# Kernel tuning notes

Hardware: AMD Instinct MI355X
Metric: run time of the kernel (lower is better)

Reference implementation:

```python
import jax, jax.numpy as jnp
import numpy as np

N, E, R = 50000, 500000, 3
IN, HID, OUT = 128, 128, 128
NEG_SLOPE = 0.2


def setup_inputs() -> dict:
    key = jax.random.key(0)
    ks = jax.random.split(key, 16)
    g = lambda i, shape: jax.random.normal(ks[i], shape, jnp.float32) * 0.1
    return {
        "x": jax.random.normal(ks[0], (N, IN), jnp.float32),
        "edge_index": jax.random.randint(ks[1], (2, E), 0, N, jnp.int32),
        "edge_type": jax.random.randint(ks[2], (E,), 0, R, jnp.int32),
        "edge_attr": jax.random.normal(ks[3], (E, 1), jnp.float32),
        # conv1 params (RGATConv: per-relation weight, q/k/e attention vectors, edge lin, bias)
        "w1": g(4, (R, IN, HID)), "q1": g(5, (HID, 1)), "k1": g(6, (HID, 1)),
        "le1": g(7, (1, HID)), "e1": g(8, (HID, 1)), "b1": jnp.zeros((HID,), jnp.float32),
        # conv2 params
        "w2": g(9, (R, HID, OUT)), "q2": g(10, (OUT, 1)), "k2": g(11, (OUT, 1)),
        "le2": g(12, (1, OUT)), "e2": g(13, (OUT, 1)), "b2": jnp.zeros((OUT,), jnp.float32),
    }


def _rgat_conv(x, src, dst, edge_type, edge_attr, w, q, k, le, e, b):
    """PyG RGATConv: heads=1, dim=1, additive-self-attention, across-relation softmax."""
    n = x.shape[0]
    # Per-relation linear at node level (equiv. to per-edge bmm with w[edge_type])
    xw = jnp.einsum('ni,rio->rno', x, w)            # [R, N, C]
    x_j = xw[edge_type, src]                          # [E, C] transformed source feats
    x_i = xw[edge_type, dst]                          # [E, C] transformed target feats
    # additive attention logits: q(x_i) + k(x_j) + e(lin_edge(edge_attr))
    alpha = x_i @ q + x_j @ k + (edge_attr @ le) @ e  # [E, 1]
    alpha = jax.nn.leaky_relu(alpha, negative_slope=NEG_SLOPE)
    # across-relation softmax over incoming edges of each target node
    amax = jax.ops.segment_max(alpha, dst, num_segments=n)
    amax = jnp.where(jnp.isfinite(amax), amax, 0.0)   # empty segments -> 0
    ex = jnp.exp(alpha - amax[dst])
    denom = jax.ops.segment_sum(ex, dst, num_segments=n)
    alpha = ex / (denom[dst] + 1e-16)
    # weighted scatter-add aggregation, then bias (concat=True, heads=1)
    out = jax.ops.segment_sum(alpha * x_j, dst, num_segments=n)  # [N, C]
    return out + b


def reference(x, edge_index, edge_type, edge_attr,
              w1, q1, k1, le1, e1, b1,
              w2, q2, k2, le2, e2, b2):
    src, dst = edge_index[0], edge_index[1]
    h = jax.nn.relu(_rgat_conv(x, src, dst, edge_type, edge_attr, w1, q1, k1, le1, e1, b1))
    return _rgat_conv(h, src, dst, edge_type, edge_attr, w2, q2, k2, le2, e2, b2)
```

## Files before the change

### kernel.cpp

```cpp
#include <hip/hip_runtime.h>
#include <hip/hip_bf16.h>
#include <math.h>

typedef __bf16 bf16x8 __attribute__((ext_vector_type(8)));
typedef float f32x4 __attribute__((ext_vector_type(4)));

#define CDIM 128

__global__ void sentinel_kernel(float* outf) {
  if (threadIdx.x == 0) outf[0] = 12345.0f;
}

__global__ __launch_bounds__(256) void prep_kernel(
    const float* __restrict__ w1, const float* __restrict__ w2,
    __hip_bfloat16* __restrict__ wt,
    const float* __restrict__ le1, const float* __restrict__ e1,
    const float* __restrict__ le2, const float* __restrict__ e2,
    float* __restrict__ outc, int* __restrict__ deg, int perW, int n) {
  const int b = blockIdx.x;
  const int tid = threadIdx.x;
  if (b < 48) {
    int t = b * 256 + tid;
    if (t >= perW * 2) return;
    const float* w = (t < perW) ? w1 : w2;
    int tt = (t < perW) ? t : t - perW;
    int r = tt >> 11;
    int rem = tt & 2047;
    int kb = rem >> 7;
    int o = rem & 127;
    const float* wr = w + ((size_t)r << 14);
    union { __hip_bfloat16 h[8]; int4 v; } u;
#pragma unroll
    for (int j = 0; j < 8; ++j)
      u.h[j] = __float2bfloat16(wr[(size_t)(kb * 8 + j) * CDIM + o]);
    *reinterpret_cast<int4*>(wt + (size_t)t * 8) = u.v;
  } else if (b == 48) {
    if (tid < 64) {
      float v1 = le1[tid] * e1[tid] + le1[tid + 64] * e1[tid + 64];
      float v2 = le2[tid] * e2[tid] + le2[tid + 64] * e2[tid + 64];
#pragma unroll
      for (int off = 32; off > 0; off >>= 1) {
        v1 += __shfl_xor(v1, off, 64);
        v2 += __shfl_xor(v2, off, 64);
      }
      if (tid == 0) { outc[0] = v1; outc[1] = v2; }
    }
  } else {
    int i = (b - 49) * 256 + tid;
    if (i < n) deg[i] = 0;
  }
}


__global__ __launch_bounds__(256) void hist_kernel(const int* __restrict__ dstv,
                                                   int* __restrict__ deg, int E) {
  int e = blockIdx.x * 256 + threadIdx.x;
  if (e < E) atomicAdd(&deg[dstv[e]], 1);
}

__global__ __launch_bounds__(256) void scan1_kernel(const int* __restrict__ deg,
                                                    int* __restrict__ rowptr,
                                                    int* __restrict__ partials, int n) {
  __shared__ int sh[256];
  int t = threadIdx.x;
  int base = blockIdx.x * 1024;
  int idx = base + t * 4;
  int v[4]; int s = 0;
#pragma unroll
  for (int j = 0; j < 4; ++j) { v[j] = (idx + j < n) ? deg[idx + j] : 0; s += v[j]; }
  sh[t] = s;
  __syncthreads();
  for (int off = 1; off < 256; off <<= 1) {
    int x = (t >= off) ? sh[t - off] : 0;
    __syncthreads();
    sh[t] += x;
    __syncthreads();
  }
  int excl = sh[t] - s;
  if (t == 255) partials[blockIdx.x] = sh[255];
  int run = excl;
#pragma unroll
  for (int j = 0; j < 4; ++j) {
    if (idx + j < n) rowptr[idx + j] = run;
    run += v[j];
  }
}

__global__ __launch_bounds__(256) void scan3_kernel(int* __restrict__ rowptr,
                                                    int* __restrict__ cursor,
                                                    const int* __restrict__ partials,
                                                    int nb, int n, int E) {
  __shared__ int spfx[64];
  int t = threadIdx.x;
  if (t < 64) {
    int pv = (t < nb) ? partials[t] : 0;
    int v = pv;
#pragma unroll
    for (int off = 1; off < 64; off <<= 1) {
      int u = __shfl_up(v, off, 64);
      if (t >= off) v += u;
    }
    spfx[t] = v - pv;
  }
  __syncthreads();
  int i = blockIdx.x * 256 + t;
  if (i < n) {
    int v = rowptr[i] + spfx[i >> 10];
    rowptr[i] = v;
    cursor[i] = v;
  } else if (i == n) {
    rowptr[n] = E;
  }
}

__global__ __launch_bounds__(256) void scatter_kernel(
    const int* __restrict__ srcv, const int* __restrict__ dstv,
    const int* __restrict__ etype, const float* __restrict__ eattr,
    int* __restrict__ cursor, int2* __restrict__ kattr, int E, int n) {
  int e = blockIdx.x * 256 + threadIdx.x;
  if (e >= E) return;
  int p = atomicAdd(&cursor[dstv[e]], 1);
  kattr[p] = make_int2(etype[e] * n + srcv[e], __float_as_int(eattr[e]));
}

__global__ __launch_bounds__(256) void gemm_xw_kernel(
    const float* __restrict__ xin, const __hip_bfloat16* __restrict__ wt,
    const float* __restrict__ qv, const float* __restrict__ kv,
    __hip_bfloat16* __restrict__ xwout, float* __restrict__ sq, float* __restrict__ sk,
    int n) {
  __shared__ __hip_bfloat16 wlds[16 * 128 * 8];
  __shared__ float qls[128], kls[128];
  const int base = blockIdx.x * 64;
  const int tid = threadIdx.x;
  const int wave = tid >> 6, lane = tid & 63;
  const int quad = lane >> 4, c16 = lane & 15;

  if (tid < 128) qls[tid] = qv[tid];
  else kls[tid - 128] = kv[tid - 128];

  bf16x8 zf;
#pragma unroll
  for (int j = 0; j < 8; ++j) zf[j] = (__bf16)0.0f;

  const int m = base + wave * 16 + c16;
  const bool ok = m < n;
  bf16x8 af[4];
#pragma unroll
  for (int ks = 0; ks < 4; ++ks) {
    if (ok) {
      const float* xp = xin + (size_t)m * CDIM + ks * 32 + quad * 8;
      f32x4 x0 = *reinterpret_cast<const f32x4*>(xp);
      f32x4 x1 = *reinterpret_cast<const f32x4*>(xp + 4);
      bf16x8 a;
#pragma unroll
      for (int j = 0; j < 4; ++j) { a[j] = (__bf16)x0[j]; a[4 + j] = (__bf16)x1[j]; }
      af[ks] = a;
    } else {
      af[ks] = zf;
    }
  }

  for (int r = 0; r < 3; ++r) {
    if (r) __syncthreads();
    {
      const int4* src = reinterpret_cast<const int4*>(wt + ((size_t)r << 14));
      int4* dst = reinterpret_cast<int4*>(wlds);
#pragma unroll
      for (int i = 0; i < 8; ++i) dst[tid + i * 256] = src[tid + i * 256];
    }
    __syncthreads();

    f32x4 acc[8];
#pragma unroll
    for (int ot = 0; ot < 8; ++ot) acc[ot] = (f32x4){0.f, 0.f, 0.f, 0.f};

#pragma unroll
    for (int ks = 0; ks < 4; ++ks) {
#pragma unroll
      for (int ot = 0; ot < 8; ++ot) {
        bf16x8 b = *reinterpret_cast<const bf16x8*>(
            &wlds[(((ks * 4 + quad) * 128) + ot * 16 + c16) * 8]);
        acc[ot] = __builtin_amdgcn_mfma_f32_16x16x32_bf16(b, af[ks], acc[ot], 0, 0, 0);
      }
    }

    __hip_bfloat16* rp = xwout + (((size_t)r * n + m) << 7) + quad * 4;
    float s_q = 0.f, s_k = 0.f;
#pragma unroll
    for (int ot = 0; ot < 8; ++ot) {
      f32x4 a = acc[ot];
      f32x4 q4 = *reinterpret_cast<const f32x4*>(&qls[ot * 16 + quad * 4]);
      f32x4 k4 = *reinterpret_cast<const f32x4*>(&kls[ot * 16 + quad * 4]);
      s_q += a[0] * q4[0] + a[1] * q4[1] + a[2] * q4[2] + a[3] * q4[3];
      s_k += a[0] * k4[0] + a[1] * k4[1] + a[2] * k4[2] + a[3] * k4[3];
      if (ok) {
        union { __hip_bfloat16 b4[4]; uint2 u; } pk;
#pragma unroll
        for (int t = 0; t < 4; ++t) pk.b4[t] = __float2bfloat16(a[t]);
        *reinterpret_cast<uint2*>(rp + ot * 16) = pk.u;
      }
    }
    s_q += __shfl_xor(s_q, 16, 64);
    s_q += __shfl_xor(s_q, 32, 64);
    s_k += __shfl_xor(s_k, 16, 64);
    s_k += __shfl_xor(s_k, 32, 64);
    if (quad == 0 && ok) {
      sq[(size_t)r * n + m] = s_q;
      sk[(size_t)r * n + m] = s_k;
    }
  }
}

__global__ __launch_bounds__(256) void aggregate_kernel(
    const int* __restrict__ rowptr, const int2* __restrict__ kattr,
    const float* __restrict__ sq, const float* __restrict__ sk,
    const __hip_bfloat16* __restrict__ xw, const float* __restrict__ bias,
    const float* __restrict__ cscal, float* __restrict__ out, int n, int do_relu) {
  const int wave = threadIdx.x >> 6, lane = threadIdx.x & 63;
  const int node = blockIdx.x * 4 + wave;
  if (node >= n) return;
  const int g = lane >> 4;
  const int sub = lane & 15;
  const float c = cscal[0];
  const int n2 = n * 2;

  const int start = rowptr[node];
  const int deg = rowptr[node + 1] - start;
  const float s0 = sq[node], s1 = sq[n + node], s2 = sq[n2 + node];

  float acc[8];
#pragma unroll
  for (int t = 0; t < 8; ++t) acc[t] = 0.f;
  float den = 0.f;

  for (int j0 = 0; j0 < deg; j0 += 16) {
    const int jb = j0 + (g << 2);
    int2 ka[4];
#pragma unroll
    for (int t = 0; t < 4; ++t) {
      int idx = jb + t;
      ka[t] = kattr[start + (idx < deg ? idx : 0)];
    }
    float w[4];
    bf16x8 f[4];
#pragma unroll
    for (int t = 0; t < 4; ++t) {
      int kk = ka[t].x;
      float sv = (kk >= n2) ? s2 : ((kk >= n) ? s1 : s0);
      float l = sv + sk[kk] + c * __int_as_float(ka[t].y);
      l = l > 0.f ? l : 0.2f * l;
      w[t] = (jb + t < deg) ? __expf(l) : 0.f;
      f[t] = *reinterpret_cast<const bf16x8*>(xw + ((size_t)kk << 7) + sub * 8);
    }
#pragma unroll
    for (int t = 0; t < 8; ++t)
      acc[t] += w[0] * (float)f[0][t] + w[1] * (float)f[1][t] +
                w[2] * (float)f[2][t] + w[3] * (float)f[3][t];
    den += (w[0] + w[1]) + (w[2] + w[3]);
  }

#pragma unroll
  for (int t = 0; t < 8; ++t) {
    acc[t] += __shfl_xor(acc[t], 16, 64);
    acc[t] += __shfl_xor(acc[t], 32, 64);
  }
  den += __shfl_xor(den, 16, 64);
  den += __shfl_xor(den, 32, 64);

  if (g == 0) {
    float inv = 1.0f / (den + 1e-16f);
    f32x4 b0 = *reinterpret_cast<const f32x4*>(bias + sub * 8);
    f32x4 b1 = *reinterpret_cast<const f32x4*>(bias + sub * 8 + 4);
    f32x4 o0, o1;
#pragma unroll
    for (int t = 0; t < 4; ++t) {
      o0[t] = acc[t] * inv + b0[t];
      o1[t] = acc[4 + t] * inv + b1[t];
    }
    if (do_relu) {
#pragma unroll
      for (int t = 0; t < 4; ++t) {
        o0[t] = fmaxf(o0[t], 0.f);
        o1[t] = fmaxf(o1[t], 0.f);
      }
    }
    float* op = out + (size_t)node * CDIM + sub * 8;
    *reinterpret_cast<f32x4*>(op) = o0;
    *reinterpret_cast<f32x4*>(op + 4) = o1;
  }
}


extern "C" void kernel_launch(void* const* d_in, const int* in_sizes, int n_in,
                              void* d_out, int out_size, void* d_ws, size_t ws_size,
                              hipStream_t stream) {
  const float* x     = (const float*)d_in[0];
  const int*   eidx  = (const int*)d_in[1];
  const int*   etype = (const int*)d_in[2];
  const float* eattr = (const float*)d_in[3];
  const float* w1  = (const float*)d_in[4];
  const float* q1  = (const float*)d_in[5];
  const float* k1  = (const float*)d_in[6];
  const float* le1 = (const float*)d_in[7];
  const float* e1  = (const float*)d_in[8];
  const float* b1  = (const float*)d_in[9];
  const float* w2  = (const float*)d_in[10];
  const float* q2  = (const float*)d_in[11];
  const float* k2  = (const float*)d_in[12];
  const float* le2 = (const float*)d_in[13];
  const float* e2  = (const float*)d_in[14];
  const float* b2  = (const float*)d_in[15];

  const int N = in_sizes[0] / CDIM;
  const int E = in_sizes[2];
  const int R = in_sizes[4] / (CDIM * CDIM);
  const int* srcv = eidx;
  const int* dstv = eidx + E;

  char* p = (char*)d_ws;
  auto alloc = [&](size_t bytes) -> void* {
    void* q = (void*)p;
    p += (bytes + 255) & ~(size_t)255;
    return q;
  };
  float* sq       = (float*)alloc((size_t)R * N * 4);
  float* sk       = (float*)alloc((size_t)R * N * 4);
  int*   deg      = (int*)alloc((size_t)N * 4);
  int*   rowptr   = (int*)alloc((size_t)(N + 1) * 4);
  int*   cursor   = (int*)alloc((size_t)N * 4);
  int*   partials = (int*)alloc(4096);
  int2*  kattr    = (int2*)alloc((size_t)E * 8);
  __hip_bfloat16* wt = (__hip_bfloat16*)alloc((size_t)2 * R * CDIM * CDIM * 2);
  float* cscal    = (float*)alloc(256);
  __hip_bfloat16* xw = (__hip_bfloat16*)alloc((size_t)R * N * CDIM * 2);

  size_t needed = (size_t)(p - (char*)d_ws);
  if (needed > ws_size) {
    sentinel_kernel<<<1, 64, 0, stream>>>((float*)d_out);
    return;
  }

  float* outp = (float*)d_out;
  float* hbuf = outp;

  const int eg = (E + 255) / 256;
  const int nb = (N + 1023) / 1024;
  const int nodes4 = (N + 3) / 4;
  const int perW = R * 2048;
  const int prep_grid = 49 + (N + 255) / 256;

  prep_kernel<<<prep_grid, 256, 0, stream>>>(w1, w2, wt, le1, e1, le2, e2,
                                             cscal, deg, perW, N);

  hist_kernel<<<eg, 256, 0, stream>>>(dstv, deg, E);
  scan1_kernel<<<nb, 256, 0, stream>>>(deg, rowptr, partials, N);
  scan3_kernel<<<(N + 1 + 255) / 256, 256, 0, stream>>>(rowptr, cursor, partials, nb, N, E);
  scatter_kernel<<<eg, 256, 0, stream>>>(srcv, dstv, etype, eattr, cursor, kattr, E, N);

  dim3 ggrid((N + 63) / 64);

  gemm_xw_kernel<<<ggrid, 256, 0, stream>>>(x, wt, q1, k1, xw, sq, sk, N);
  aggregate_kernel<<<nodes4, 256, 0, stream>>>(rowptr, kattr, sq, sk, xw, b1,
                                               cscal + 0, hbuf, N, 1);

  gemm_xw_kernel<<<ggrid, 256, 0, stream>>>(hbuf, wt + (size_t)R * CDIM * CDIM,
                                            q2, k2, xw, sq, sk, N);
  aggregate_kernel<<<nodes4, 256, 0, stream>>>(rowptr, kattr, sq, sk, xw, b2,
                                               cscal + 1, outp, N, 0);
}
```

Before: 270.5 us.

## Fuse whole two-layer RGAT pipeline into one cooperative persistent megakernel

Replaces the sequence of separate launches (prep, histogram, scans, scatter, GEMMs, aggregations) with a single cooperative kernel that uses grid-wide syncs between phases and atomic work counters for dynamic scheduling. It also overlaps the degree histogram with the first-layer GEMM in the same work queue. The aim is to remove per-launch overhead and idle gaps between small kernels. In exchange, grid syncs cost time, occupancy is capped by cooperative launch limits, and the host now makes several attribute and occupancy queries on every call. The old multi-kernel path is kept as a fallback.

Measured after the change: 774.0 us. 2.86x slower.

```diff
diff --git a/kernel.cpp b/kernel.cpp
--- a/kernel.cpp
+++ b/kernel.cpp
@@ -1,6 +1,9 @@
 #include <hip/hip_runtime.h>
 #include <hip/hip_bf16.h>
+#include <hip/hip_cooperative_groups.h>
 #include <math.h>
+
+namespace cg = cooperative_groups;
 
 typedef __bf16 bf16x8 __attribute__((ext_vector_type(8)));
 typedef float f32x4 __attribute__((ext_vector_type(4)));
@@ -10,6 +13,7 @@
 __global__ void sentinel_kernel(float* outf) {
   if (threadIdx.x == 0) outf[0] = 12345.0f;
 }
+
 
 __global__ __launch_bounds__(256) void prep_kernel(
     const float* __restrict__ w1, const float* __restrict__ w2,
@@ -51,7 +55,6 @@
   }
 }
 
-
 __global__ __launch_bounds__(256) void hist_kernel(const int* __restrict__ dstv,
                                                    int* __restrict__ deg, int E) {
   int e = blockIdx.x * 256 + threadIdx.x;
@@ -287,6 +290,371 @@
     float* op = out + (size_t)node * CDIM + sub * 8;
     *reinterpret_cast<f32x4*>(op) = o0;
     *reinterpret_cast<f32x4*>(op + 4) = o1;
+  }
+}
+
+
+struct MP {
+  const float* x;
+  const int* srcv; const int* dstv; const int* etype; const float* eattr;
+  const float* w1; const float* q1; const float* k1;
+  const float* le1; const float* e1; const float* b1;
+  const float* w2; const float* q2; const float* k2;
+  const float* le2; const float* e2; const float* b2;
+  float* sq; float* sk;
+  int* deg; int* rowptr; int* cursor; int* partials;
+  int2* kattr; __hip_bfloat16* wt; float* cscal; __hip_bfloat16* xw;
+  float* hbuf; float* outp; int* ctrs;
+  int N, E;
+};
+
+__device__ __forceinline__ void gemm_tile(
+    int tb, const float* __restrict__ xin, const __hip_bfloat16* __restrict__ wtL,
+    const float* qls, const float* kls, __hip_bfloat16* wlds,
+    __hip_bfloat16* __restrict__ xwout, float* __restrict__ sq,
+    float* __restrict__ sk, int n) {
+  const int tid = threadIdx.x;
+  const int wave = tid >> 6, lane = tid & 63;
+  const int quad = lane >> 4, c16 = lane & 15;
+  const int m = tb * 64 + wave * 16 + c16;
+  const bool ok = m < n;
+
+  bf16x8 zf;
+#pragma unroll
+  for (int j = 0; j < 8; ++j) zf[j] = (__bf16)0.0f;
+
+  bf16x8 af[4];
+#pragma unroll
+  for (int ks = 0; ks < 4; ++ks) {
+    if (ok) {
+      const float* xp = xin + (size_t)m * CDIM + ks * 32 + quad * 8;
+      f32x4 x0 = *reinterpret_cast<const f32x4*>(xp);
+      f32x4 x1 = *reinterpret_cast<const f32x4*>(xp + 4);
+      bf16x8 a;
+#pragma unroll
+      for (int j = 0; j < 4; ++j) { a[j] = (__bf16)x0[j]; a[4 + j] = (__bf16)x1[j]; }
+      af[ks] = a;
+    } else {
+      af[ks] = zf;
+    }
+  }
+
+  for (int r = 0; r < 3; ++r) {
+    __syncthreads();
+    {
+      const int4* src = reinterpret_cast<const int4*>(wtL + ((size_t)r << 14));
+      int4* dst = reinterpret_cast<int4*>(wlds);
+#pragma unroll
+      for (int i = 0; i < 8; ++i) dst[tid + i * 256] = src[tid + i * 256];
+    }
+    __syncthreads();
+
+    f32x4 acc[8];
+#pragma unroll
+    for (int ot = 0; ot < 8; ++ot) acc[ot] = (f32x4){0.f, 0.f, 0.f, 0.f};
+
+#pragma unroll
+    for (int ks = 0; ks < 4; ++ks) {
+#pragma unroll
+      for (int ot = 0; ot < 8; ++ot) {
+        bf16x8 b = *reinterpret_cast<const bf16x8*>(
+            &wlds[(((ks * 4 + quad) * 128) + ot * 16 + c16) * 8]);
+        acc[ot] = __builtin_amdgcn_mfma_f32_16x16x32_bf16(b, af[ks], acc[ot], 0, 0, 0);
+      }
+    }
+
+    __hip_bfloat16* rp = xwout + (((size_t)r * n + m) << 7) + quad * 4;
+    float s_q = 0.f, s_k = 0.f;
+#pragma unroll
+    for (int ot = 0; ot < 8; ++ot) {
+      f32x4 a = acc[ot];
+      f32x4 q4 = *reinterpret_cast<const f32x4*>(&qls[ot * 16 + quad * 4]);
+      f32x4 k4 = *reinterpret_cast<const f32x4*>(&kls[ot * 16 + quad * 4]);
+      s_q += a[0] * q4[0] + a[1] * q4[1] + a[2] * q4[2] + a[3] * q4[3];
+      s_k += a[0] * k4[0] + a[1] * k4[1] + a[2] * k4[2] + a[3] * k4[3];
+      if (ok) {
+        union { __hip_bfloat16 b4[4]; uint2 u; } pk;
+#pragma unroll
+        for (int t = 0; t < 4; ++t) pk.b4[t] = __float2bfloat16(a[t]);
+        *reinterpret_cast<uint2*>(rp + ot * 16) = pk.u;
+      }
+    }
+    s_q += __shfl_xor(s_q, 16, 64);
+    s_q += __shfl_xor(s_q, 32, 64);
+    s_k += __shfl_xor(s_k, 16, 64);
+    s_k += __shfl_xor(s_k, 32, 64);
+    if (quad == 0 && ok) {
+      sq[(size_t)r * n + m] = s_q;
+      sk[(size_t)r * n + m] = s_k;
+    }
+  }
+}
+
+__device__ __forceinline__ void agg_unit(
+    int u, const int* __restrict__ rowptr, const int2* __restrict__ kattr,
+    const float* __restrict__ sq, const float* __restrict__ sk,
+    const __hip_bfloat16* __restrict__ xw, const float* __restrict__ bias,
+    float c, float* __restrict__ out, int n, int do_relu) {
+  const int wave = threadIdx.x >> 6, lane = threadIdx.x & 63;
+  const int g = lane >> 4;
+  const int sub = lane & 15;
+  const int n2 = n * 2;
+
+#pragma unroll
+  for (int ii = 0; ii < 4; ++ii) {
+    const int node = u * 16 + wave * 4 + ii;
+    if (node >= n) continue;
+
+    const int start = rowptr[node];
+    const int deg = rowptr[node + 1] - start;
+    const float s0 = sq[node], s1 = sq[n + node], s2 = sq[n2 + node];
+
+    float acc[8];
+#pragma unroll
+    for (int t = 0; t < 8; ++t) acc[t] = 0.f;
+    float den = 0.f;
+
+    for (int j0 = 0; j0 < deg; j0 += 16) {
+      const int jb = j0 + (g << 2);
+      int2 ka[4];
+#pragma unroll
+      for (int t = 0; t < 4; ++t) {
+        int idx = jb + t;
+        ka[t] = kattr[start + (idx < deg ? idx : 0)];
+      }
+      float w[4];
+      bf16x8 f[4];
+#pragma unroll
+      for (int t = 0; t < 4; ++t) {
+        int kk = ka[t].x;
+        float sv = (kk >= n2) ? s2 : ((kk >= n) ? s1 : s0);
+        float l = sv + sk[kk] + c * __int_as_float(ka[t].y);
+        l = l > 0.f ? l : 0.2f * l;
+        w[t] = (jb + t < deg) ? __expf(l) : 0.f;
+        f[t] = *reinterpret_cast<const bf16x8*>(xw + ((size_t)kk << 7) + sub * 8);
+      }
+#pragma unroll
+      for (int t = 0; t < 8; ++t)
+        acc[t] += w[0] * (float)f[0][t] + w[1] * (float)f[1][t] +
+                  w[2] * (float)f[2][t] + w[3] * (float)f[3][t];
+      den += (w[0] + w[1]) + (w[2] + w[3]);
+    }
+
+#pragma unroll
+    for (int t = 0; t < 8; ++t) {
+      acc[t] += __shfl_xor(acc[t], 16, 64);
+      acc[t] += __shfl_xor(acc[t], 32, 64);
+    }
+    den += __shfl_xor(den, 16, 64);
+    den += __shfl_xor(den, 32, 64);
+
+    if (g == 0) {
+      float inv = 1.0f / (den + 1e-16f);
+      f32x4 b0 = *reinterpret_cast<const f32x4*>(bias + sub * 8);
+      f32x4 b1 = *reinterpret_cast<const f32x4*>(bias + sub * 8 + 4);
+      f32x4 o0, o1;
+#pragma unroll
+      for (int t = 0; t < 4; ++t) {
+        o0[t] = acc[t] * inv + b0[t];
+        o1[t] = acc[4 + t] * inv + b1[t];
+      }
+      if (do_relu) {
+#pragma unroll
+        for (int t = 0; t < 4; ++t) {
+          o0[t] = fmaxf(o0[t], 0.f);
+          o1[t] = fmaxf(o1[t], 0.f);
+        }
+      }
+      float* op = out + (size_t)node * CDIM + sub * 8;
+      *reinterpret_cast<f32x4*>(op) = o0;
+      *reinterpret_cast<f32x4*>(op + 4) = o1;
+    }
+  }
+}
+
+__global__ __launch_bounds__(256, 4) void mega_kernel(MP p) {
+  cg::grid_group grid = cg::this_grid();
+  __shared__ __hip_bfloat16 wlds[16 * 128 * 8];
+  __shared__ float qls[128], kls[128];
+  __shared__ int ssc[256];
+  __shared__ int sChunk;
+
+  const int tid = threadIdx.x;
+  const int bid = blockIdx.x;
+  const int gsz = gridDim.x * 256;
+  const int gtid = bid * 256 + tid;
+  const int N = p.N, E = p.E;
+  const int NT = (N + 63) >> 6;
+  const int NH = (E + 2047) >> 11;
+  const int NU = (N + 15) >> 4;
+  const int nbp = (N + 1023) >> 10;
+
+  {
+    const int perW = 3 * 2048;
+    for (int t = gtid; t < perW * 2; t += gsz) {
+      const float* w = (t < perW) ? p.w1 : p.w2;
+      int tt = (t < perW) ? t : t - perW;
+      int r = tt >> 11, rem = tt & 2047, kb = rem >> 7, o = rem & 127;
+      const float* wr = w + ((size_t)r << 14);
+      union { __hip_bfloat16 h[8]; int4 v; } u;
+#pragma unroll
+      for (int j = 0; j < 8; ++j)
+        u.h[j] = __float2bfloat16(wr[(size_t)(kb * 8 + j) * CDIM + o]);
+      *reinterpret_cast<int4*>(p.wt + (size_t)t * 8) = u.v;
+    }
+    for (int i = gtid; i < N; i += gsz) p.deg[i] = 0;
+    if (bid == 0 && tid < 64) {
+      float v1 = p.le1[tid] * p.e1[tid] + p.le1[tid + 64] * p.e1[tid + 64];
+      float v2 = p.le2[tid] * p.e2[tid] + p.le2[tid + 64] * p.e2[tid + 64];
+#pragma unroll
+      for (int off = 32; off > 0; off >>= 1) {
+        v1 += __shfl_xor(v1, off, 64);
+        v2 += __shfl_xor(v2, off, 64);
+      }
+      if (tid == 0) { p.cscal[0] = v1; p.cscal[1] = v2; }
+    }
+    if (bid == 0 && tid == 0) {
+#pragma unroll
+      for (int i = 0; i < 8; ++i) p.ctrs[i] = 0;
+    }
+  }
+  grid.sync();
+
+  if (tid < 128) qls[tid] = p.q1[tid];
+  else kls[tid - 128] = p.k1[tid - 128];
+  for (;;) {
+    if (tid == 0) {
+      int c = atomicAdd(&p.ctrs[0], 1);
+      if (c < NH) sChunk = c;
+      else {
+        int t2 = atomicAdd(&p.ctrs[1], 1);
+        sChunk = (t2 < NT) ? (100000 + t2) : -1;
+      }
+    }
+    __syncthreads();
+    int c = sChunk;
+    __syncthreads();
+    if (c < 0) break;
+    if (c < 100000) {
+      int e0 = c << 11;
+      int e1e = e0 + 2048 < E ? e0 + 2048 : E;
+      for (int e = e0 + tid; e < e1e; e += 256) atomicAdd(&p.deg[p.dstv[e]], 1);
+    } else {
+      gemm_tile(c - 100000, p.x, p.wt, qls, kls, wlds, p.xw, p.sq, p.sk, N);
+    }
+  }
+  grid.sync();
+
+  if (bid < nbp) {
+    int base1 = bid << 10;
+    int idx = base1 + tid * 4;
+    int v[4]; int s = 0;
+#pragma unroll
+    for (int j = 0; j < 4; ++j) { v[j] = (idx + j < N) ? p.deg[idx + j] : 0; s += v[j]; }
+    ssc[tid] = s;
+    __syncthreads();
+    for (int off = 1; off < 256; off <<= 1) {
+      int x = (tid >= off) ? ssc[tid - off] : 0;
+      __syncthreads();
+      ssc[tid] += x;
+      __syncthreads();
+    }
+    int excl = ssc[tid] - s;
+    if (tid == 255) p.partials[bid] = ssc[255];
+    int run = excl;
+#pragma unroll
+    for (int j = 0; j < 4; ++j) {
+      if (idx + j < N) p.rowptr[idx + j] = run;
+      run += v[j];
+    }
+  }
+  grid.sync();
+
+  if (bid < ((N + 1 + 255) >> 8)) {
+    if (tid < 64) {
+      int pv = (tid < nbp) ? p.partials[tid] : 0;
+      int v = pv;
+#pragma unroll
+      for (int off = 1; off < 64; off <<= 1) {
+        int u = __shfl_up(v, off, 64);
+        if (tid >= off) v += u;
+      }
+      ssc[tid] = v - pv;
+    }
+    __syncthreads();
+    int i = bid * 256 + tid;
+    if (i < N) {
+      int v = p.rowptr[i] + ssc[i >> 10];
+      p.rowptr[i] = v;
+      p.cursor[i] = v;
+    } else if (i == N) {
+      p.rowptr[N] = E;
+    }
+  }
+  grid.sync();
+
+  for (;;) {
+    if (tid == 0) {
+      int c = atomicAdd(&p.ctrs[2], 1);
+      sChunk = (c < NH) ? c : -1;
+    }
+    __syncthreads();
+    int c = sChunk;
+    __syncthreads();
+    if (c < 0) break;
+    int e0 = c << 11;
+    int e1e = e0 + 2048 < E ? e0 + 2048 : E;
+    for (int e = e0 + tid; e < e1e; e += 256) {
+      int pdx = atomicAdd(&p.cursor[p.dstv[e]], 1);
+      p.kattr[pdx] = make_int2(p.etype[e] * N + p.srcv[e], __float_as_int(p.eattr[e]));
+    }
+  }
+  grid.sync();
+
+  {
+    const float cv = p.cscal[0];
+    for (;;) {
+      if (tid == 0) {
+        int c = atomicAdd(&p.ctrs[3], 1);
+        sChunk = (c < NU) ? c : -1;
+      }
+      __syncthreads();
+      int u = sChunk;
+      __syncthreads();
+      if (u < 0) break;
+      agg_unit(u, p.rowptr, p.kattr, p.sq, p.sk, p.xw, p.b1, cv, p.hbuf, N, 1);
+    }
+  }
+  grid.sync();
+
+  if (tid < 128) qls[tid] = p.q2[tid];
+  else kls[tid - 128] = p.k2[tid - 128];
+  for (;;) {
+    if (tid == 0) {
+      int t2 = atomicAdd(&p.ctrs[4], 1);
+      sChunk = (t2 < NT) ? t2 : -1;
+    }
+    __syncthreads();
+    int t2 = sChunk;
+    __syncthreads();
+    if (t2 < 0) break;
+    gemm_tile(t2, p.hbuf, p.wt + 3 * CDIM * CDIM, qls, kls, wlds, p.xw, p.sq, p.sk, N);
+  }
+  grid.sync();
+
+  {
+    const float cv = p.cscal[1];
+    for (;;) {
+      if (tid == 0) {
+        int c = atomicAdd(&p.ctrs[5], 1);
+        sChunk = (c < NU) ? c : -1;
+      }
+      __syncthreads();
+      int u = sChunk;
+      __syncthreads();
+      if (u < 0) break;
+      agg_unit(u, p.rowptr, p.kattr, p.sq, p.sk, p.xw, p.b2, cv, p.outp, N, 0);
+    }
   }
 }
 
@@ -332,6 +700,7 @@
   int2*  kattr    = (int2*)alloc((size_t)E * 8);
   __hip_bfloat16* wt = (__hip_bfloat16*)alloc((size_t)2 * R * CDIM * CDIM * 2);
   float* cscal    = (float*)alloc(256);
+  int*   ctrs     = (int*)alloc(256);
   __hip_bfloat16* xw = (__hip_bfloat16*)alloc((size_t)R * N * CDIM * 2);
 
   size_t needed = (size_t)(p - (char*)d_ws);
@@ -342,6 +711,36 @@
 
   float* outp = (float*)d_out;
   float* hbuf = outp;
+
+  {
+    int dev = 0;
+    (void)hipGetDevice(&dev);
+    int coop = 0;
+    (void)hipDeviceGetAttribute(&coop, hipDeviceAttributeCooperativeLaunch, dev);
+    int ncu = 0;
+    (void)hipDeviceGetAttribute(&ncu, hipDeviceAttributeMultiprocessorCount, dev);
+    int maxb = 0;
+    if (hipOccupancyMaxActiveBlocksPerMultiprocessor(&maxb, mega_kernel, 256, 0) !=
+        hipSuccess)
+      maxb = 0;
+    long nblocks = (long)maxb * (long)(ncu > 0 ? ncu : 0);
+    if (nblocks > 1024) nblocks = 1024;
+    if (coop && nblocks >= 256) {
+      MP mp;
+      mp.x = x; mp.srcv = srcv; mp.dstv = dstv; mp.etype = etype; mp.eattr = eattr;
+      mp.w1 = w1; mp.q1 = q1; mp.k1 = k1; mp.le1 = le1; mp.e1 = e1; mp.b1 = b1;
+      mp.w2 = w2; mp.q2 = q2; mp.k2 = k2; mp.le2 = le2; mp.e2 = e2; mp.b2 = b2;
+      mp.sq = sq; mp.sk = sk; mp.deg = deg; mp.rowptr = rowptr; mp.cursor = cursor;
+      mp.partials = partials; mp.kattr = kattr; mp.wt = wt; mp.cscal = cscal;
+      mp.xw = xw; mp.hbuf = hbuf; mp.outp = outp; mp.ctrs = ctrs;
+      mp.N = N; mp.E = E;
+      void* args[] = {&mp};
+      hipError_t rc = hipLaunchCooperativeKernel((const void*)mega_kernel,
+                                                 dim3((unsigned)nblocks), dim3(256),
+                                                 args, 0, stream);
+      if (rc == hipSuccess) return;
+    }
+  }
 
   const int eg = (E + 255) / 256;
   const int nb = (N + 1023) / 1024;
```
